# Performance work log

Hardware: AMD Instinct MI355X
Metric: run time of the kernel (lower is better)

The kernel has to match this reference:

```python
import jax, jax.numpy as jnp
import numpy as np

B, S, H = 2, 4096, 2048
NH, NKV, HD = 16, 4, 128          # heads, kv heads, head_dim = H // NH
GS_RATIO = 0.25                    # hardcoded in MyAttention.forward
ROPE_BASE = 10000.0


def rotate_half(x):
    h = x.shape[-1] // 2
    return jnp.concatenate((-x[..., h:], x[..., :h]), axis=-1)


def setup_inputs() -> dict:
    key = jax.random.key(0)
    ks = jax.random.split(key, 5)
    g = int(S * GS_RATIO)
    hidden_states = jax.random.normal(ks[0], (B, S, H), jnp.float32)
    position_ids = jnp.tile(jnp.arange(S, dtype=jnp.int32)[None, :], (B, 1))
    # causal additive mask per group window (0 keep, -1e9 masked)
    i = jnp.arange(g)
    causal = i[None, :] <= i[:, None]
    attention_mask = jnp.broadcast_to(
        jnp.where(causal, 0.0, -1e9).astype(jnp.float32)[None, None], (B, 1, g, g)
    )
    sc = 0.02
    Wq = (jax.random.normal(ks[1], (H, NH * HD), jnp.float32) * sc)
    Wk = (jax.random.normal(ks[2], (H, NKV * HD), jnp.float32) * sc)
    Wv = (jax.random.normal(ks[3], (H, NKV * HD), jnp.float32) * sc)
    Wo = (jax.random.normal(ks[4], (NH * HD, H), jnp.float32) * sc)
    return {"hidden_states": hidden_states, "attention_mask": attention_mask,
            "position_ids": position_ids, "Wq": Wq, "Wk": Wk, "Wv": Wv, "Wo": Wo}


def reference(hidden_states, attention_mask, position_ids, Wq, Wk, Wv, Wo):
    B_, S_, H_ = hidden_states.shape
    g = int(S_ * GS_RATIO)
    ng = S_ // g
    n_rep = NH // NKV

    # QKV projections -> (B, heads, S, HD)
    q = (hidden_states @ Wq).reshape(B_, S_, NH, HD).transpose(0, 2, 1, 3)
    k = (hidden_states @ Wk).reshape(B_, S_, NKV, HD).transpose(0, 2, 1, 3)
    v = (hidden_states @ Wv).reshape(B_, S_, NKV, HD).transpose(0, 2, 1, 3)

    # RoPE
    inv_freq = 1.0 / (ROPE_BASE ** (jnp.arange(0, HD, 2, dtype=jnp.float32) / HD))
    t = jnp.arange(S_, dtype=jnp.float32)
    emb = jnp.concatenate([jnp.outer(t, inv_freq)] * 2, axis=-1)  # (S, HD)
    cos = jnp.cos(emb)[position_ids][:, None]  # (B,1,S,HD)
    sin = jnp.sin(emb)[position_ids][:, None]
    q = q * cos + rotate_half(q) * sin
    k = k * cos + rotate_half(k) * sin

    # GQA repeat_kv
    k = jnp.repeat(k, n_rep, axis=1)
    v = jnp.repeat(v, n_rep, axis=1)

    # S2-Attn shift: roll second half of heads by -g/2 along seq, then group
    def shift(x):
        x = jnp.concatenate([x[:, :NH // 2],
                             jnp.roll(x[:, NH // 2:], -g // 2, axis=2)], axis=1)
        return x.transpose(0, 2, 1, 3).reshape(B_ * ng, g, NH, HD).transpose(0, 2, 1, 3)

    q, k, v = shift(q), shift(k), shift(v)

    attn = jnp.einsum('bhqd,bhkd->bhqk', q, k) / np.float32(np.sqrt(HD))
    mask = jnp.tile(attention_mask, (ng, 1, 1, 1))  # (B*ng,1,g,g)
    attn = attn + mask
    attn = jax.nn.softmax(attn.astype(jnp.float32), axis=-1).astype(q.dtype)

    out = jnp.einsum('bhqk,bhkd->bhqd', attn, v)  # (B*ng, NH, g, HD)
    out = out.transpose(0, 2, 1, 3).reshape(B_, S_, NH, HD)
    # undo shift for second half of heads (+g/2 along seq)
    out = jnp.concatenate([out[:, :, :NH // 2],
                           jnp.roll(out[:, :, NH // 2:], g // 2, axis=1)], axis=2)
    out = out.reshape(B_, S_, NH * HD) @ Wo
    return out
```

## Files before the change

kernel.cpp:

```cpp
#include <hip/hip_runtime.h>
#include <math.h>

typedef unsigned short u16;
typedef short bf16x8 __attribute__((ext_vector_type(8)));
typedef float f32x4 __attribute__((ext_vector_type(4)));


__device__ __forceinline__ u16 f2bf(float x) {
  union { float f; unsigned u; } c; c.f = x;
  unsigned r = (c.u + 0x7FFFu + ((c.u >> 16) & 1u)) >> 16;
  return (u16)r;
}
__device__ __forceinline__ float bf2f(u16 x) {
  union { unsigned u; float f; } c; c.u = ((unsigned)x) << 16;
  return c.f;
}

#define GLD16(gp, lp)                                                   \
  __builtin_amdgcn_global_load_lds(                                     \
      (__attribute__((address_space(1))) void*)(gp),                    \
      (__attribute__((address_space(3))) void*)(lp), 16, 0, 0)

__global__ __launch_bounds__(256) void cast_bf16_vec(
    const float* __restrict__ X, u16* __restrict__ Y) {
  const size_t i = ((size_t)blockIdx.x * 256 + threadIdx.x) * 4;
  float4 v = *(const float4*)(X + i);
  ushort4 o;
  o.x = f2bf(v.x); o.y = f2bf(v.y); o.z = f2bf(v.z); o.w = f2bf(v.w);
  *(ushort4*)(Y + i) = o;
}

__global__ __launch_bounds__(256) void wt_cast(
    const float* __restrict__ W, u16* __restrict__ Wt, int K, int N) {
  const int bk = blockIdx.y * 64;
  const int bn = blockIdx.x * 64;
  __shared__ float T[64 * 65];
  const int tid = threadIdx.x;
  #pragma unroll
  for (int u = 0; u < 16; ++u) {
    int idx = tid + u * 256;
    int kl = idx >> 6, nl = idx & 63;
    T[kl * 65 + nl] = W[(size_t)(bk + kl) * N + bn + nl];
  }
  __syncthreads();
  #pragma unroll
  for (int u = 0; u < 16; ++u) {
    int idx = tid + u * 256;
    int nl = idx >> 6, kl = idx & 63;
    Wt[(size_t)(bn + nl) * K + bk + kl] = f2bf(T[kl * 65 + nl]);
  }
}

__global__ __launch_bounds__(256) void gemm_bf16(
    const u16* __restrict__ A, const u16* __restrict__ Bt,
    float* __restrict__ Cf, u16* __restrict__ Cb, int M, int N, int K) {
  __shared__ u16 As[128 * 32];
  __shared__ u16 Bs[128 * 32];

  const int tid = threadIdx.x;
  const int bm = blockIdx.y * 128;
  const int bn = blockIdx.x * 128;
  const int w = tid >> 6, lane = tid & 63;
  const int col = lane & 15, quad = lane >> 4;
  const int mblk = (w & 1) * 64, nblk = (w >> 1) * 64;

  const int srow = tid >> 2;
  const int sseg = (tid & 3) * 8;

  const u16* ag0 = A + (size_t)(bm + srow) * K + sseg;
  const u16* ag1 = A + (size_t)(bm + 64 + srow) * K + sseg;
  const u16* bg0 = Bt + (size_t)(bn + srow) * K + sseg;
  const u16* bg1 = Bt + (size_t)(bn + 64 + srow) * K + sseg;
  u16* al = &As[srow * 32 + sseg];
  u16* bl = &Bs[srow * 32 + sseg];

  f32x4 acc[4][4];
  #pragma unroll
  for (int i = 0; i < 4; ++i)
    #pragma unroll
    for (int j = 0; j < 4; ++j) acc[i][j] = (f32x4)(0.0f);

  for (int k0 = 0; k0 < K; k0 += 32) {
    __syncthreads();
    GLD16(ag0 + k0, al);
    GLD16(ag1 + k0, al + 64 * 32);
    GLD16(bg0 + k0, bl);
    GLD16(bg1 + k0, bl + 64 * 32);
    __syncthreads();

    bf16x8 af[4], bfr[4];
    #pragma unroll
    for (int i = 0; i < 4; ++i)
      af[i] = *(const bf16x8*)&As[(mblk + 16 * i + col) * 32 + quad * 8];
    #pragma unroll
    for (int j = 0; j < 4; ++j)
      bfr[j] = *(const bf16x8*)&Bs[(nblk + 16 * j + col) * 32 + quad * 8];
    #pragma unroll
    for (int i = 0; i < 4; ++i)
      #pragma unroll
      for (int j = 0; j < 4; ++j)
        acc[i][j] = __builtin_amdgcn_mfma_f32_16x16x32_bf16(af[i], bfr[j], acc[i][j], 0, 0, 0);
  }

  #pragma unroll
  for (int i = 0; i < 4; ++i) {
    const int row0 = bm + mblk + 16 * i + quad * 4;
    #pragma unroll
    for (int j = 0; j < 4; ++j) {
      const int cc = bn + nblk + 16 * j + col;
      #pragma unroll
      for (int r = 0; r < 4; ++r) {
        if (Cb) Cb[(size_t)(row0 + r) * N + cc] = f2bf(acc[i][j][r]);
        else    Cf[(size_t)(row0 + r) * N + cc] = acc[i][j][r];
      }
    }
  }
}

__global__ __launch_bounds__(256) void rope_qkv(
    u16* __restrict__ QKV, const int* __restrict__ pos) {
  const unsigned idx = blockIdx.x * 256 + threadIdx.x;
  const int d = idx & 63;
  const unsigned rest = idx >> 6;
  const int hh = rest % 20;
  const unsigned bs = rest / 20;

  const int colbase = (hh < 16) ? hh * 128 : 2048 + (hh - 16) * 128;
  u16* p = QKV + (size_t)bs * 3072 + colbase + d;
  const float x0 = bf2f(p[0]);
  const float x1 = bf2f(p[64]);
  const float t = (float)pos[bs];
  const float inv_freq = __expf((float)d * -0.14391156509676332f);
  float s, c;
  __sincosf(t * inv_freq, &s, &c);
  const float sc = (hh < 16) ? 0.08838834764831845f : 1.0f;
  p[0]  = f2bf((x0 * c - x1 * s) * sc);
  p[64] = f2bf((x1 * c + x0 * s) * sc);
}

__global__ __launch_bounds__(256) void v_transpose(
    const u16* __restrict__ QKV, u16* __restrict__ Vt) {
  const int bid = blockIdx.x;
  const int st = bid & 63;
  const int kvh = (bid >> 6) & 3;
  const int b = bid >> 8;
  __shared__ u16 T[64 * 136];
  const int tid = threadIdx.x;
  #pragma unroll
  for (int u = 0; u < 4; ++u) {
    int idx = tid + u * 256;
    int sl = idx >> 4, ch = idx & 15;
    *(uint4*)&T[sl * 136 + ch * 8] =
        *(const uint4*)(QKV + ((size_t)(b * 4096 + st * 64 + sl)) * 3072 + 2560 + kvh * 128 + ch * 8);
  }
  __syncthreads();
  #pragma unroll
  for (int u = 0; u < 32; ++u) {
    int idx = tid + u * 256;
    int d = idx >> 6, sl = idx & 63;
    Vt[((size_t)((b * 4 + kvh) * 128 + d)) * 4096 + st * 64 + sl] = T[sl * 136 + d];
  }
}

__global__ __launch_bounds__(256) void attn_mfma(
    const u16* __restrict__ QKV, const u16* __restrict__ Vt,
    u16* __restrict__ Ob) {
  __shared__ u16 Ks[64 * 136];
  __shared__ u16 Vs[128 * 72];
  __shared__ u16 Ps[4][16 * 72];

  const int bid = blockIdx.x;
  const int qt = 15 - (bid & 15);
  const int h  = (bid >> 4) & 15;
  const int gi = (bid >> 8) & 3;
  const int b  = bid >> 10;

  const int tid = threadIdx.x;
  const int w = tid >> 6, lane = tid & 63;
  const int col = lane & 15, quad = lane >> 4;

  const int shift = (h >= 8) ? 512 : 0;
  const int base_s = gi * 1024;
  const int kvh = h >> 2;

  const int sq0 = (base_s + qt * 64 + shift) & 4095;
  {
    const u16* qsrc = QKV + ((size_t)(b * 4096 + sq0)) * 3072 + h * 128;
    #pragma unroll
    for (int u = 0; u < 4; ++u) {
      int idx = tid + u * 256;
      int row = idx >> 4, ch = idx & 15;
      *(uint4*)&Ks[row * 136 + ch * 8] =
          *(const uint4*)(qsrc + (size_t)row * 3072 + ch * 8);
    }
  }
  __syncthreads();
  bf16x8 aq[4];
  #pragma unroll
  for (int kk = 0; kk < 4; ++kk)
    aq[kk] = *(const bf16x8*)&Ks[(w * 16 + col) * 136 + kk * 32 + quad * 8];

  f32x4 o[8];
  #pragma unroll
  for (int jd = 0; jd < 8; ++jd) o[jd] = (f32x4)(0.0f);
  float lp[4] = {0.0f, 0.0f, 0.0f, 0.0f};

  u16* Pw = &Ps[w][0];
  const int qrow_l = w * 16 + quad * 4;

  for (int kt = 0; kt <= qt; ++kt) {
    const int sk0 = (base_s + kt * 64 + shift) & 4095;
    __syncthreads();
    {
      const u16* ksrc = QKV + ((size_t)(b * 4096 + sk0)) * 3072 + 2048 + kvh * 128;
      #pragma unroll
      for (int u = 0; u < 4; ++u) {
        int idx = tid + u * 256;
        int row = idx >> 4, ch = idx & 15;
        *(uint4*)&Ks[row * 136 + ch * 8] =
            *(const uint4*)(ksrc + (size_t)row * 3072 + ch * 8);
      }
      const u16* vsrc = Vt + ((size_t)((b * 4 + kvh) * 128)) * 4096 + sk0;
      #pragma unroll
      for (int u = 0; u < 4; ++u) {
        int idx = tid + u * 256;
        int d = idx >> 3, ch = idx & 7;
        *(uint4*)&Vs[d * 72 + ch * 8] =
            *(const uint4*)(vsrc + (size_t)d * 4096 + ch * 8);
      }
    }
    __syncthreads();

    f32x4 sc[4];
    #pragma unroll
    for (int j = 0; j < 4; ++j) sc[j] = (f32x4)(0.0f);
    #pragma unroll
    for (int kk = 0; kk < 4; ++kk) {
      #pragma unroll
      for (int j = 0; j < 4; ++j) {
        bf16x8 bk = *(const bf16x8*)&Ks[(16 * j + col) * 136 + kk * 32 + quad * 8];
        sc[j] = __builtin_amdgcn_mfma_f32_16x16x32_bf16(aq[kk], bk, sc[j], 0, 0, 0);
      }
    }

    #pragma unroll
    for (int j = 0; j < 4; ++j) {
      #pragma unroll
      for (int r = 0; r < 4; ++r) {
        float p = __expf(sc[j][r]);
        if (kt == qt && (16 * j + col) > (qrow_l + r)) p = 0.0f;
        lp[r] += p;
        Pw[(quad * 4 + r) * 72 + 16 * j + col] = f2bf(p);
      }
    }

    #pragma unroll
    for (int ks = 0; ks < 2; ++ks) {
      bf16x8 ap = *(const bf16x8*)&Pw[col * 72 + ks * 32 + quad * 8];
      #pragma unroll
      for (int jd = 0; jd < 8; ++jd) {
        bf16x8 bv = *(const bf16x8*)&Vs[(16 * jd + col) * 72 + ks * 32 + quad * 8];
        o[jd] = __builtin_amdgcn_mfma_f32_16x16x32_bf16(ap, bv, o[jd], 0, 0, 0);
      }
    }
  }

  #pragma unroll
  for (int r = 0; r < 4; ++r) {
    lp[r] += __shfl_xor(lp[r], 1, 64);
    lp[r] += __shfl_xor(lp[r], 2, 64);
    lp[r] += __shfl_xor(lp[r], 4, 64);
    lp[r] += __shfl_xor(lp[r], 8, 64);
  }

  #pragma unroll
  for (int r = 0; r < 4; ++r) {
    const int qg = qt * 64 + w * 16 + quad * 4 + r;
    const int sq = (base_s + qg + shift) & 4095;
    u16* dst = Ob + ((size_t)(b * 4096 + sq)) * 2048 + h * 128;
    const float inv = 1.0f / lp[r];
    #pragma unroll
    for (int jd = 0; jd < 8; ++jd)
      dst[16 * jd + col] = f2bf(o[jd][r] * inv);
  }
}

extern "C" void kernel_launch(void* const* d_in, const int* in_sizes, int n_in,
                              void* d_out, int out_size, void* d_ws, size_t ws_size,
                              hipStream_t stream) {
  const float* hs = (const float*)d_in[0];
  const int*   pos = (const int*)d_in[2];
  const float* Wq = (const float*)d_in[3];
  const float* Wk = (const float*)d_in[4];
  const float* Wv = (const float*)d_in[5];
  const float* Wo = (const float*)d_in[6];

  char* ws = (char*)d_ws;
  u16* hsb   = (u16*)ws; ws += (size_t)8192 * 2048 * 2;
  u16* Wqkvt = (u16*)ws; ws += (size_t)3072 * 2048 * 2;
  u16* Wot   = (u16*)ws; ws += (size_t)2048 * 2048 * 2;
  u16* QKVb  = (u16*)ws; ws += (size_t)8192 * 3072 * 2;
  u16* Vtt   = (u16*)ws; ws += (size_t)2 * 4 * 128 * 4096 * 2;
  u16* Obh   = (u16*)ws; ws += (size_t)8192 * 2048 * 2;

  dim3 blk(256);

  cast_bf16_vec<<<16384, blk, 0, stream>>>(hs, hsb);
  wt_cast<<<dim3(32, 32), blk, 0, stream>>>(Wq, Wqkvt, 2048, 2048);
  wt_cast<<<dim3(8, 32),  blk, 0, stream>>>(Wk, Wqkvt + (size_t)2048 * 2048, 2048, 512);
  wt_cast<<<dim3(8, 32),  blk, 0, stream>>>(Wv, Wqkvt + (size_t)2560 * 2048, 2048, 512);
  wt_cast<<<dim3(32, 32), blk, 0, stream>>>(Wo, Wot, 2048, 2048);

  gemm_bf16<<<dim3(24, 64), blk, 0, stream>>>(hsb, Wqkvt, nullptr, QKVb, 8192, 3072, 2048);

  rope_qkv<<<40960, blk, 0, stream>>>(QKVb, pos);

  v_transpose<<<512, blk, 0, stream>>>(QKVb, Vtt);

  attn_mfma<<<2048, blk, 0, stream>>>(QKVb, Vtt, Obh);

  gemm_bf16<<<dim3(16, 64), blk, 0, stream>>>(Obh, Wot, (float*)d_out, nullptr, 8192, 2048, 2048);
}
```

Measured before the change: 568.9 us.

## Double attention query tile to 128 rows with register-prefetched K/V tiles

The attention kernel now runs 512-thread blocks that each cover 128 query rows, so each K/V tile loaded into shared memory serves twice as many queries and the grid is halved. The next K/V tile is prefetched into registers while the current tile is being computed. Q fragments are loaded straight from global memory instead of going through shared memory. The causal-mask check now runs only on the last two diagonal tiles. In exchange the kernel uses more registers, and the coarser tiles increase load imbalance across the causal triangle.

```diff
diff --git a/kernel.cpp b/kernel.cpp
--- a/kernel.cpp
+++ b/kernel.cpp
@@ -162,18 +162,18 @@
   }
 }
 
-__global__ __launch_bounds__(256) void attn_mfma(
+__global__ __launch_bounds__(512, 4) void attn_mfma(
     const u16* __restrict__ QKV, const u16* __restrict__ Vt,
     u16* __restrict__ Ob) {
   __shared__ u16 Ks[64 * 136];
   __shared__ u16 Vs[128 * 72];
-  __shared__ u16 Ps[4][16 * 72];
+  __shared__ u16 Ps[8][16 * 72];
 
   const int bid = blockIdx.x;
-  const int qt = 15 - (bid & 15);
-  const int h  = (bid >> 4) & 15;
-  const int gi = (bid >> 8) & 3;
-  const int b  = bid >> 10;
+  const int qt = 7 - (bid & 7);
+  const int h  = (bid >> 3) & 15;
+  const int gi = (bid >> 7) & 3;
+  const int b  = bid >> 9;
 
   const int tid = threadIdx.x;
   const int w = tid >> 6, lane = tid & 63;
@@ -182,23 +182,32 @@
   const int shift = (h >= 8) ? 512 : 0;
   const int base_s = gi * 1024;
   const int kvh = h >> 2;
-
-  const int sq0 = (base_s + qt * 64 + shift) & 4095;
+  const int ktmax = 2 * qt + 1;
+
+  const int krow = tid >> 4, kch = tid & 15;
+  const int vrow = tid >> 3, vch = tid & 7;
+
+  const u16* ksrc = QKV + ((size_t)(b * 4096)) * 3072 + 2048 + kvh * 128;
+  const u16* vsrc = Vt + ((size_t)((b * 4 + kvh) * 128)) * 4096;
+
+  uint4 kreg[2], vreg[2];
   {
-    const u16* qsrc = QKV + ((size_t)(b * 4096 + sq0)) * 3072 + h * 128;
-    #pragma unroll
-    for (int u = 0; u < 4; ++u) {
-      int idx = tid + u * 256;
-      int row = idx >> 4, ch = idx & 15;
-      *(uint4*)&Ks[row * 136 + ch * 8] =
-          *(const uint4*)(qsrc + (size_t)row * 3072 + ch * 8);
-    }
-  }
-  __syncthreads();
+    const int sk0 = (base_s + shift) & 4095;
+    kreg[0] = *(const uint4*)(ksrc + (size_t)(sk0 + krow) * 3072 + kch * 8);
+    kreg[1] = *(const uint4*)(ksrc + (size_t)(sk0 + 32 + krow) * 3072 + kch * 8);
+    vreg[0] = *(const uint4*)(vsrc + (size_t)vrow * 4096 + sk0 + vch * 8);
+    vreg[1] = *(const uint4*)(vsrc + (size_t)(64 + vrow) * 4096 + sk0 + vch * 8);
+  }
+
   bf16x8 aq[4];
-  #pragma unroll
-  for (int kk = 0; kk < 4; ++kk)
-    aq[kk] = *(const bf16x8*)&Ks[(w * 16 + col) * 136 + kk * 32 + quad * 8];
+  {
+    const int qg = qt * 128 + w * 16 + col;
+    const int sqr = (base_s + qg + shift) & 4095;
+    const u16* qp = QKV + ((size_t)(b * 4096 + sqr)) * 3072 + h * 128;
+    #pragma unroll
+    for (int kk = 0; kk < 4; ++kk)
+      aq[kk] = *(const bf16x8*)(qp + kk * 32 + quad * 8);
+  }
 
   f32x4 o[8];
   #pragma unroll
@@ -206,30 +215,23 @@
   float lp[4] = {0.0f, 0.0f, 0.0f, 0.0f};
 
   u16* Pw = &Ps[w][0];
-  const int qrow_l = w * 16 + quad * 4;
-
-  for (int kt = 0; kt <= qt; ++kt) {
-    const int sk0 = (base_s + kt * 64 + shift) & 4095;
+  const int qrow_l = qt * 128 + w * 16 + quad * 4;
+
+  for (int kt = 0; kt <= ktmax; ++kt) {
     __syncthreads();
-    {
-      const u16* ksrc = QKV + ((size_t)(b * 4096 + sk0)) * 3072 + 2048 + kvh * 128;
-      #pragma unroll
-      for (int u = 0; u < 4; ++u) {
-        int idx = tid + u * 256;
-        int row = idx >> 4, ch = idx & 15;
-        *(uint4*)&Ks[row * 136 + ch * 8] =
-            *(const uint4*)(ksrc + (size_t)row * 3072 + ch * 8);
-      }
-      const u16* vsrc = Vt + ((size_t)((b * 4 + kvh) * 128)) * 4096 + sk0;
-      #pragma unroll
-      for (int u = 0; u < 4; ++u) {
-        int idx = tid + u * 256;
-        int d = idx >> 3, ch = idx & 7;
-        *(uint4*)&Vs[d * 72 + ch * 8] =
-            *(const uint4*)(vsrc + (size_t)d * 4096 + ch * 8);
-      }
-    }
+    *(uint4*)&Ks[krow * 136 + kch * 8] = kreg[0];
+    *(uint4*)&Ks[(32 + krow) * 136 + kch * 8] = kreg[1];
+    *(uint4*)&Vs[vrow * 72 + vch * 8] = vreg[0];
+    *(uint4*)&Vs[(64 + vrow) * 72 + vch * 8] = vreg[1];
     __syncthreads();
+
+    if (kt < ktmax) {
+      const int skn = (base_s + (kt + 1) * 64 + shift) & 4095;
+      kreg[0] = *(const uint4*)(ksrc + (size_t)(skn + krow) * 3072 + kch * 8);
+      kreg[1] = *(const uint4*)(ksrc + (size_t)(skn + 32 + krow) * 3072 + kch * 8);
+      vreg[0] = *(const uint4*)(vsrc + (size_t)vrow * 4096 + skn + vch * 8);
+      vreg[1] = *(const uint4*)(vsrc + (size_t)(64 + vrow) * 4096 + skn + vch * 8);
+    }
 
     f32x4 sc[4];
     #pragma unroll
@@ -243,14 +245,26 @@
       }
     }
 
-    #pragma unroll
-    for (int j = 0; j < 4; ++j) {
-      #pragma unroll
-      for (int r = 0; r < 4; ++r) {
-        float p = __expf(sc[j][r]);
-        if (kt == qt && (16 * j + col) > (qrow_l + r)) p = 0.0f;
-        lp[r] += p;
-        Pw[(quad * 4 + r) * 72 + 16 * j + col] = f2bf(p);
+    if (kt >= 2 * qt) {
+      #pragma unroll
+      for (int j = 0; j < 4; ++j) {
+        #pragma unroll
+        for (int r = 0; r < 4; ++r) {
+          float p = __expf(sc[j][r]);
+          if ((kt * 64 + 16 * j + col) > (qrow_l + r)) p = 0.0f;
+          lp[r] += p;
+          Pw[(quad * 4 + r) * 72 + 16 * j + col] = f2bf(p);
+        }
+      }
+    } else {
+      #pragma unroll
+      for (int j = 0; j < 4; ++j) {
+        #pragma unroll
+        for (int r = 0; r < 4; ++r) {
+          float p = __expf(sc[j][r]);
+          lp[r] += p;
+          Pw[(quad * 4 + r) * 72 + 16 * j + col] = f2bf(p);
+        }
       }
     }
 
@@ -275,7 +289,7 @@
 
   #pragma unroll
   for (int r = 0; r < 4; ++r) {
-    const int qg = qt * 64 + w * 16 + quad * 4 + r;
+    const int qg = qt * 128 + w * 16 + quad * 4 + r;
     const int sq = (base_s + qg + shift) & 4095;
     u16* dst = Ob + ((size_t)(b * 4096 + sq)) * 2048 + h * 128;
     const float inv = 1.0f / lp[r];
@@ -314,10 +328,9 @@
   gemm_bf16<<<dim3(24, 64), blk, 0, stream>>>(hsb, Wqkvt, nullptr, QKVb, 8192, 3072, 2048);
 
   rope_qkv<<<40960, blk, 0, stream>>>(QKVb, pos);
-
   v_transpose<<<512, blk, 0, stream>>>(QKVb, Vtt);
 
-  attn_mfma<<<2048, blk, 0, stream>>>(QKVb, Vtt, Obh);
+  attn_mfma<<<1024, dim3(512), 0, stream>>>(QKVb, Vtt, Obh);
 
   gemm_bf16<<<dim3(16, 64), blk, 0, stream>>>(Obh, Wot, (float*)d_out, nullptr, 8192, 2048, 2048);
 }
```

Result: slower. 606.6 us (+6.6%).
